# Kernel optimization log

Measured on AMD Instinct MI355X. Metric: run time of the kernel, lower is better.

The kernel has to match this reference:

```python
import jax, jax.numpy as jnp
import numpy as np

B_, L_, DM = 8, 1024, 256
DS, DC, EX = 16, 4, 2
DI = EX * DM            # d_inner = 512
DTR = max(1, DM // 16)  # dt_rank = 16


def setup_inputs() -> dict:
    key = jax.random.key(0)
    ks = iter(jax.random.split(key, 40))
    def n(shape, s=0.02):
        return jax.random.normal(next(ks), shape, jnp.float32) * s
    inp = {"x": jax.random.normal(next(ks), (B_, L_, DM), jnp.float32)}
    inp["norm_g"] = jnp.ones((DM,), jnp.float32)
    inp["norm_b"] = jnp.zeros((DM,), jnp.float32)
    for m in ("f", "b"):
        inp[f"inW_{m}"] = n((DM, 2 * DI))
        inp[f"convW_{m}"] = n((DI, DC))
        inp[f"convB_{m}"] = jnp.zeros((DI,), jnp.float32)
        inp[f"xW_{m}"] = n((DI, DTR + 2 * DS))
        inp[f"dtW_{m}"] = n((DTR, DI))
        inp[f"dtB_{m}"] = jnp.zeros((DI,), jnp.float32)
        # ALog init: log of [1..dState] repeated over dInner rows
        inp[f"ALog_{m}"] = jnp.log(jnp.tile(jnp.arange(1, DS + 1, dtype=jnp.float32), (DI, 1)))
        inp[f"Dp_{m}"] = jnp.ones((DI,), jnp.float32)
        inp[f"outW_{m}"] = n((DI, DM))
    inp["fusW"] = n((2 * DM, DM))
    inp["fusB"] = jnp.zeros((DM,), jnp.float32)
    return inp


def _dw_conv(x, w, b):
    # causal depthwise conv1d: x [B,L,DI], w [DI,DC] -> [B,L,DI]
    xc = jnp.transpose(x, (0, 2, 1))  # B,DI,L
    out = jax.lax.conv_general_dilated(
        xc, w[:, None, :], window_strides=(1,), padding=[(DC - 1, 0)],
        dimension_numbers=("NCH", "OIH", "NCH"), feature_group_count=DI)
    return jnp.transpose(out + b[:, None], (0, 2, 1))


def _ssm(x, xW, dtW, dtB, ALog, Dp):
    # x: [B,L,DI]
    A = -jnp.exp(ALog)                                   # [DI,DS]
    xdbl = x @ xW                                        # [B,L,DTR+2*DS]
    dlt, Bp, Cp = jnp.split(xdbl, [DTR, DTR + DS], axis=-1)
    delta = jax.nn.softplus(dlt @ dtW + dtB)             # [B,L,DI]
    dA = jnp.exp(delta[..., None] * A)                   # [B,L,DI,DS]
    dBx = (delta * x)[..., None] * Bp[:, :, None, :]     # [B,L,DI,DS]

    def step(h, t):
        a, bb, c = t
        h = a * h + bb                                   # [B,DI,DS]
        y = jnp.einsum('bdn,bn->bd', h, c)
        return h, y

    h0 = jnp.zeros((x.shape[0], DI, DS), x.dtype)
    _, ys = jax.lax.scan(step, h0, (jnp.moveaxis(dA, 1, 0),
                                    jnp.moveaxis(dBx, 1, 0),
                                    jnp.moveaxis(Cp, 1, 0)))
    return jnp.moveaxis(ys, 0, 1) + Dp * x               # [B,L,DI]


def _mamba(x, inW, convW, convB, xW, dtW, dtB, ALog, Dp, outW):
    xr = x @ inW                                         # [B,L,2*DI]
    xs, res = jnp.split(xr, 2, axis=-1)
    xs = jax.nn.silu(_dw_conv(xs, convW, convB))
    y = _ssm(xs, xW, dtW, dtB, ALog, Dp)
    return (y * jax.nn.silu(res)) @ outW                 # [B,L,DM]


def reference(x, norm_g, norm_b,
              inW_f, convW_f, convB_f, xW_f, dtW_f, dtB_f, ALog_f, Dp_f, outW_f,
              inW_b, convW_b, convB_b, xW_b, dtW_b, dtB_b, ALog_b, Dp_b, outW_b,
              fusW, fusB):
    # LayerNorm
    mu = x.mean(-1, keepdims=True)
    var = ((x - mu) ** 2).mean(-1, keepdims=True)
    xn = (x - mu) * jax.lax.rsqrt(var + 1e-5) * norm_g + norm_b
    # forward-direction Mamba
    xf = _mamba(xn, inW_f, convW_f, convB_f, xW_f, dtW_f, dtB_f, ALog_f, Dp_f, outW_f)
    # backward-direction Mamba (flip along time)
    xb = _mamba(jnp.flip(xn, 1), inW_b, convW_b, convB_b, xW_b, dtW_b, dtB_b, ALog_b, Dp_b, outW_b)
    xb = jnp.flip(xb, 1)
    fused = jnp.concatenate([xf, xb], axis=-1) @ fusW + fusB
    return x + fused  # dropout is identity in eval
```

## Files before the change

### kernel.cpp

```cpp
#include <hip/hip_runtime.h>
#include <cmath>

typedef __bf16 bf16x8 __attribute__((ext_vector_type(8)));
typedef float  f32x4  __attribute__((ext_vector_type(4)));
typedef float  f32x2  __attribute__((ext_vector_type(2)));

#define B_  8
#define L_  1024
#define DM  256
#define DI  512
#define DS  16
#define DTR 16
#define M_  (B_*L_)
#define NC  64
#define CT  16

__device__ inline float softplus_f(float z){
  return (z > 20.f) ? z : __logf(1.f + __expf(z));
}
__device__ inline float silu_f(float z){
  return z / (1.f + __expf(-z));
}

__device__ inline void pow_tree(float e1, float* p){
  float e2=e1*e1, e4=e2*e2, e8=e4*e4;
  float e3=e2*e1, e5=e4*e1, e6=e4*e2, e7=e4*e3;
  p[0]=e1;  p[1]=e2;  p[2]=e3;  p[3]=e4;
  p[4]=e5;  p[5]=e6;  p[6]=e7;  p[7]=e8;
  p[8]=e8*e1;  p[9]=e8*e2;  p[10]=e8*e3;  p[11]=e8*e4;
  p[12]=e8*e5; p[13]=e8*e6; p[14]=e8*e7;  p[15]=e8*e8;
}

__device__ inline int flag_from_x(const void* x){
  const unsigned short* u = (const unsigned short*)x;
  int lane = threadIdx.x & 63;
  unsigned short v = u[2*lane];
  int e = (v >> 7) & 0xFF;
  unsigned long long m = __ballot(e >= 160 || e < 96);
  return __popcll(m) > 16;
}

struct PrepJob { const void* src; void* dst; int rows; int cols; int f32out; };
struct PrepArgs { PrepJob j[26]; int nj; };

__global__ __launch_bounds__(256) void prep_k(PrepArgs a, const void* xsrc){
  const int f = flag_from_x(xsrc);
  int e = blockIdx.x*256 + threadIdx.x;
  #pragma unroll 1
  for (int jj=0; jj<a.nj; jj++){
    int sz = a.j[jj].rows * a.j[jj].cols;
    if (e < sz){
      int cols = a.j[jj].cols;
      int r = e / cols, c = e - r*cols;
      float v = f ? ((const float*)a.j[jj].src)[e] : (float)((const __bf16*)a.j[jj].src)[e];
      if (a.j[jj].f32out) ((float*)a.j[jj].dst)[c*a.j[jj].rows + r] = v;
      else ((__bf16*)a.j[jj].dst)[(long)c*a.j[jj].rows + r] = (__bf16)v;
      return;
    }
    e -= sz;
  }
}

__global__ __launch_bounds__(256) void ln_k(const void* x, const __bf16* g,
                                            const __bf16* bb, __bf16* xn){
  const int f = flag_from_x(x);
  const int row = blockIdx.x;
  const int d = threadIdx.x;
  long idx = (long)row*DM + d;
  float v = f ? ((const float*)x)[idx] : (float)(((const __bf16*)x)[idx]);
  float s = v, q = v*v;
  #pragma unroll
  for (int off=32; off>0; off>>=1){
    s += __shfl_down(s, off);
    q += __shfl_down(q, off);
  }
  __shared__ float ss[4], sq[4];
  int w = d >> 6, ln = d & 63;
  if (ln == 0){ ss[w] = s; sq[w] = q; }
  __syncthreads();
  s = ss[0]+ss[1]+ss[2]+ss[3];
  q = sq[0]+sq[1]+sq[2]+sq[3];
  float mu  = s * (1.f/DM);
  float var = q * (1.f/DM) - mu*mu;
  float xnv = (v - mu) * rsqrtf(var + 1e-5f) * (float)g[d] + (float)bb[d];
  xn[idx] = (__bf16)xnv;
}

template<int BM,int BN,int KK>
__global__ __launch_bounds__(256) void gemm_in_k(
    const __bf16* A, const __bf16* B0, const __bf16* B1,
    __bf16* xz0, __bf16* xz1, __bf16* res0, __bf16* res1,
    int lda, int ldb)
{
  constexpr int TM = BM/2, TN = BN/2;
  constexpr int WMT = TM/16, WNT = TN/16;
  constexpr int LA = BM/64, LB = BN/64;

  const int dir = blockIdx.z;
  const __bf16* Bt = dir ? B1 : B0;
  __bf16* xz  = dir ? xz1 : xz0;
  __bf16* res = dir ? res1 : res0;
  const int tid  = threadIdx.x;
  const int lane = tid & 63;
  const int wid  = tid >> 6;
  const int wm = wid & 1;
  const int wn = wid >> 1;
  const int mBase = blockIdx.x * BM;
  const int nBase = blockIdx.y * BN;
  const int lm = lane & 15;
  const int kq = (lane >> 4) * 8;

  __shared__ __bf16 As[BM*32];
  __shared__ __bf16 Bs[BN*32];

  const __bf16* aS[LA];
  const __bf16* bS[LB];
  {
    int colk = (tid & 3) * 8;
    #pragma unroll
    for (int ld=0; ld<LA; ld++){
      int r = mBase + ld*64 + (tid >> 2);
      if (dir==1){ int b = r >> 10, t = r & (L_-1); r = (b<<10) + (L_-1-t); }
      aS[ld] = A + (long)r*lda + colk;
    }
    #pragma unroll
    for (int ld=0; ld<LB; ld++){
      int r = nBase + ld*64 + (tid >> 2);
      bS[ld] = Bt + (long)r*ldb + colk;
    }
  }

  f32x4 acc[WMT][WNT] = {};
  for (int k0=0; k0<KK; k0+=32){
    #pragma unroll
    for (int ld=0; ld<LA; ld++)
      __builtin_amdgcn_global_load_lds(
        (const __attribute__((address_space(1))) void*)(aS[ld] + k0),
        (__attribute__((address_space(3))) void*)(&As[ld*2048 + tid*8]), 16, 0, 0);
    #pragma unroll
    for (int ld=0; ld<LB; ld++)
      __builtin_amdgcn_global_load_lds(
        (const __attribute__((address_space(1))) void*)(bS[ld] + k0),
        (__attribute__((address_space(3))) void*)(&Bs[ld*2048 + tid*8]), 16, 0, 0);
    __syncthreads();
    bf16x8 af[WMT], bfr[WNT];
    #pragma unroll
    for (int i=0;i<WMT;i++) af[i]  = *(const bf16x8*)&As[(wm*TM + i*16 + lm)*32 + kq];
    #pragma unroll
    for (int j=0;j<WNT;j++) bfr[j] = *(const bf16x8*)&Bs[(wn*TN + j*16 + lm)*32 + kq];
    #pragma unroll
    for (int i=0;i<WMT;i++)
      #pragma unroll
      for (int j=0;j<WNT;j++)
        acc[i][j] = __builtin_amdgcn_mfma_f32_16x16x32_bf16(af[i], bfr[j], acc[i][j], 0,0,0);
    __syncthreads();
  }

  #pragma unroll
  for (int i=0;i<WMT;i++){
    #pragma unroll
    for (int rr=0;rr<4;rr++){
      int r = mBase + wm*TM + i*16 + (lane>>4)*4 + rr;
      #pragma unroll
      for (int j=0;j<WNT;j++){
        int c = nBase + wn*TN + j*16 + lm;
        float v = acc[i][j][rr];
        if (c < DI) xz[(long)r*DI + c] = (__bf16)v;
        else        res[(long)r*DI + (c-DI)] = (__bf16)v;
      }
    }
  }
}

template<int BM,int BN,int KK>
__global__ __launch_bounds__(256) void gemm_fin_k(
    const __bf16* Af, const __bf16* Ab,
    const __bf16* Bt0, const __bf16* Bt1,
    void* Cout, const __bf16* bias, const void* resid)
{
  constexpr int TM = BM/2, TN = BN/2;
  constexpr int WMT = TM/16, WNT = TN/16;
  constexpr int LA = BM/64, LB = BN/64;

  const int of = flag_from_x(resid);
  const int tid  = threadIdx.x;
  const int lane = tid & 63;
  const int wid  = tid >> 6;
  const int wm = wid & 1;
  const int wn = wid >> 1;
  const int mBase = blockIdx.x * BM;
  const int nBase = blockIdx.y * BN;
  const int lm = lane & 15;
  const int kq = (lane >> 4) * 8;

  __shared__ __bf16 As[BM*32];
  __shared__ __bf16 Bs[BN*32];

  f32x4 acc[WMT][WNT] = {};
  #pragma unroll 1
  for (int dd=0; dd<2; dd++){
    const __bf16* A  = dd ? Ab  : Af;
    const __bf16* Bt = dd ? Bt1 : Bt0;
    const __bf16* aS[LA];
    const __bf16* bS[LB];
    {
      int colk = (tid & 3) * 8;
      #pragma unroll
      for (int ld=0; ld<LA; ld++){
        int r = mBase + ld*64 + (tid >> 2);
        if (dd==1){ int b = r >> 10, t = r & (L_-1); r = (b<<10) + (L_-1-t); }
        aS[ld] = A + (long)r*DI + colk;
      }
      #pragma unroll
      for (int ld=0; ld<LB; ld++){
        int r = nBase + ld*64 + (tid >> 2);
        bS[ld] = Bt + (long)r*DI + colk;
      }
    }
    for (int k0=0; k0<KK; k0+=32){
      #pragma unroll
      for (int ld=0; ld<LA; ld++)
        __builtin_amdgcn_global_load_lds(
          (const __attribute__((address_space(1))) void*)(aS[ld] + k0),
          (__attribute__((address_space(3))) void*)(&As[ld*2048 + tid*8]), 16, 0, 0);
      #pragma unroll
      for (int ld=0; ld<LB; ld++)
        __builtin_amdgcn_global_load_lds(
          (const __attribute__((address_space(1))) void*)(bS[ld] + k0),
          (__attribute__((address_space(3))) void*)(&Bs[ld*2048 + tid*8]), 16, 0, 0);
      __syncthreads();
      bf16x8 af[WMT], bfr[WNT];
      #pragma unroll
      for (int i=0;i<WMT;i++) af[i]  = *(const bf16x8*)&As[(wm*TM + i*16 + lm)*32 + kq];
      #pragma unroll
      for (int j=0;j<WNT;j++) bfr[j] = *(const bf16x8*)&Bs[(wn*TN + j*16 + lm)*32 + kq];
      #pragma unroll
      for (int i=0;i<WMT;i++)
        #pragma unroll
        for (int j=0;j<WNT;j++)
          acc[i][j] = __builtin_amdgcn_mfma_f32_16x16x32_bf16(af[i], bfr[j], acc[i][j], 0,0,0);
      __syncthreads();
    }
  }

  #pragma unroll
  for (int i=0;i<WMT;i++){
    #pragma unroll
    for (int rr=0;rr<4;rr++){
      int r = mBase + wm*TM + i*16 + (lane>>4)*4 + rr;
      #pragma unroll
      for (int j=0;j<WNT;j++){
        int c = nBase + wn*TN + j*16 + lm;
        float v = acc[i][j][rr];
        float rsd = of ? ((const float*)resid)[(long)r*DM + c]
                       : (float)((const __bf16*)resid)[(long)r*DM + c];
        v += (float)bias[c] + rsd;
        if (of) ((float*)Cout)[(long)r*DM + c] = v;
        else    ((__bf16*)Cout)[(long)r*DM + c] = (__bf16)v;
      }
    }
  }
}

template<int WMT,int WNT,int BWM,int BWN,int KK>
__global__ __launch_bounds__(64*BWM*BWN) void gemm_r_k(
    const __bf16* A0, const __bf16* A1,
    const __bf16* B0, const __bf16* B1,
    __bf16* C0, __bf16* C1,
    int lda, int ldb, int ldc)
{
  const int dir = blockIdx.z;
  const __bf16* A  = dir ? A1 : A0;
  const __bf16* Bt = dir ? B1 : B0;
  __bf16* C = dir ? C1 : C0;
  const int tid  = threadIdx.x;
  const int lane = tid & 63;
  const int wid  = tid >> 6;
  const int wm = wid % BWM;
  const int wn = wid / BWM;
  const int mBase = (blockIdx.x*BWM + wm) * (WMT*16);
  const int nBase = (blockIdx.y*BWN + wn) * (WNT*16);
  const int lm = lane & 15;
  const int kq = (lane >> 4) * 8;

  long aoff[WMT];
  #pragma unroll
  for (int i=0;i<WMT;i++) aoff[i] = (long)(mBase + i*16 + lm) * lda + kq;
  long boff[WNT];
  #pragma unroll
  for (int j=0;j<WNT;j++) boff[j] = (long)(nBase + j*16 + lm) * ldb + kq;

  f32x4 acc[WMT][WNT] = {};
  #pragma unroll
  for (int k0=0; k0<KK; k0+=32){
    bf16x8 af[WMT], bfr[WNT];
    #pragma unroll
    for (int i=0;i<WMT;i++) af[i]  = *(const bf16x8*)(A  + aoff[i] + k0);
    #pragma unroll
    for (int j=0;j<WNT;j++) bfr[j] = *(const bf16x8*)(Bt + boff[j] + k0);
    #pragma unroll
    for (int i=0;i<WMT;i++)
      #pragma unroll
      for (int j=0;j<WNT;j++)
        acc[i][j] = __builtin_amdgcn_mfma_f32_16x16x32_bf16(af[i], bfr[j], acc[i][j], 0,0,0);
  }

  #pragma unroll
  for (int i=0;i<WMT;i++)
    #pragma unroll
    for (int rr=0;rr<4;rr++){
      int r = mBase + i*16 + (lane>>4)*4 + rr;
      #pragma unroll
      for (int j=0;j<WNT;j++){
        int c = nBase + j*16 + lm;
        C[(long)r*ldc + c] = (__bf16)acc[i][j][rr];
      }
    }
}

__global__ __launch_bounds__(256) void xproj_k(
    const __bf16* xs0, const __bf16* xs1,
    const __bf16* B0, const __bf16* B1,
    float* xd0, float* xd1)
{
  const int dir = blockIdx.z;
  const __bf16* A  = dir ? xs1 : xs0;
  const __bf16* Bt = dir ? B1 : B0;
  float* C = dir ? xd1 : xd0;
  const int tid  = threadIdx.x;
  const int lane = tid & 63;
  const int wid  = tid >> 6;
  const int mBase = blockIdx.x*64 + wid*16;
  const int kc = blockIdx.y * 128;
  const int lm = lane & 15;
  const int kq = (lane >> 4) * 8;

  long aoff = (long)(mBase + lm)*DI + kc + kq;
  long boff[3];
  #pragma unroll
  for (int j=0;j<3;j++) boff[j] = (long)(j*16 + lm)*DI + kc + kq;

  f32x4 acc[3] = {};
  #pragma unroll
  for (int k0=0; k0<128; k0+=32){
    bf16x8 af = *(const bf16x8*)(A + aoff + k0);
    bf16x8 bfr[3];
    #pragma unroll
    for (int j=0;j<3;j++) bfr[j] = *(const bf16x8*)(Bt + boff[j] + k0);
    #pragma unroll
    for (int j=0;j<3;j++)
      acc[j] = __builtin_amdgcn_mfma_f32_16x16x32_bf16(af, bfr[j], acc[j], 0,0,0);
  }

  #pragma unroll
  for (int rr=0;rr<4;rr++){
    int r = mBase + (lane>>4)*4 + rr;
    #pragma unroll
    for (int j=0;j<3;j++){
      int c = j*16 + lm;
      atomicAdd(&C[(long)r*48 + c], acc[j][rr]);
    }
  }
}

__global__ __launch_bounds__(256) void conv_k(
    const __bf16* xz0, const __bf16* xz1,
    const float* cw0, const float* cw1,
    const __bf16* cb0, const __bf16* cb1,
    __bf16* xs0, __bf16* xs1)
{
  const int dir = blockIdx.z;
  const __bf16* xz = dir ? xz1 : xz0;
  const float*  cw = dir ? cw1 : cw0;
  const __bf16* cb = dir ? cb1 : cb0;
  __bf16* xs = dir ? xs1 : xs0;

  int gid = blockIdx.x*256 + threadIdx.x;
  int c8 = gid & 63;
  int t  = (gid >> 6) & (L_-1);
  int b  = gid >> 16;
  int cbase = c8*8;

  float acc[8];
  bf16x8 bb = *(const bf16x8*)(cb + cbase);
  #pragma unroll
  for (int c=0;c<8;c++) acc[c] = (float)bb[c];
  #pragma unroll
  for (int j=0;j<4;j++){
    int tj = t - 3 + j;
    if (tj >= 0){
      bf16x8 xv = *(const bf16x8*)(xz + ((long)(b*L_ + tj))*DI + cbase);
      #pragma unroll
      for (int c=0;c<8;c++) acc[c] += (float)xv[c] * cw[j*DI + cbase + c];
    }
  }
  bf16x8 outv;
  #pragma unroll
  for (int c=0;c<8;c++) outv[c] = (__bf16)silu_f(acc[c]);
  *(bf16x8*)(xs + ((long)(b*L_ + t))*DI + cbase) = outv;
}

__global__ __launch_bounds__(256) void dt_k(
    const float* xd0, const float* xd1,
    const float* dw0, const float* dw1,
    const __bf16* dtB0, const __bf16* dtB1,
    float* dg0, float* dg1)
{
  const int dir = blockIdx.z;
  const float*  xd  = dir ? xd1 : xd0;
  const float*  dw  = dir ? dw1 : dw0;
  const __bf16* dtB = dir ? dtB1 : dtB0;
  float* dg = dir ? dg1 : dg0;
  const long row0 = (long)blockIdx.x * 32;
  const int tid = threadIdx.x;

  __shared__ float sdlt[32][16];
  { int e = tid*2; int r = e>>4, q = e&15;
    *(f32x2*)&sdlt[r][q] = *(const f32x2*)(xd + (row0+r)*48 + q); }

  const int d0 = tid, d1 = tid + 256;
  float dwa[16], dwb[16];
  { const f32x4* p = (const f32x4*)(dw + d0*DTR);
    #pragma unroll
    for (int q=0;q<4;q++){ f32x4 v=p[q]; dwa[q*4]=v[0]; dwa[q*4+1]=v[1]; dwa[q*4+2]=v[2]; dwa[q*4+3]=v[3]; } }
  { const f32x4* p = (const f32x4*)(dw + d1*DTR);
    #pragma unroll
    for (int q=0;q<4;q++){ f32x4 v=p[q]; dwb[q*4]=v[0]; dwb[q*4+1]=v[1]; dwb[q*4+2]=v[2]; dwb[q*4+3]=v[3]; } }
  const float b0v = (float)dtB[d0];
  const float b1v = (float)dtB[d1];
  __syncthreads();

  #pragma unroll 4
  for (int r=0;r<32;r++){
    f32x4 q0 = *(const f32x4*)&sdlt[r][0];
    f32x4 q1 = *(const f32x4*)&sdlt[r][4];
    f32x4 q2 = *(const f32x4*)&sdlt[r][8];
    f32x4 q3 = *(const f32x4*)&sdlt[r][12];
    float z0 = b0v, z1 = b1v;
    z0 += q0[0]*dwa[0]+q0[1]*dwa[1]+q0[2]*dwa[2]+q0[3]*dwa[3];
    z0 += q1[0]*dwa[4]+q1[1]*dwa[5]+q1[2]*dwa[6]+q1[3]*dwa[7];
    z0 += q2[0]*dwa[8]+q2[1]*dwa[9]+q2[2]*dwa[10]+q2[3]*dwa[11];
    z0 += q3[0]*dwa[12]+q3[1]*dwa[13]+q3[2]*dwa[14]+q3[3]*dwa[15];
    z1 += q0[0]*dwb[0]+q0[1]*dwb[1]+q0[2]*dwb[2]+q0[3]*dwb[3];
    z1 += q1[0]*dwb[4]+q1[1]*dwb[5]+q1[2]*dwb[6]+q1[3]*dwb[7];
    z1 += q2[0]*dwb[8]+q2[1]*dwb[9]+q2[2]*dwb[10]+q2[3]*dwb[11];
    z1 += q3[0]*dwb[12]+q3[1]*dwb[13]+q3[2]*dwb[14]+q3[3]*dwb[15];
    dg[(row0+r)*DI + d0] = softplus_f(z0);
    dg[(row0+r)*DI + d1] = softplus_f(z1);
  }
}

__global__ __launch_bounds__(256) void scanA_k(
    const float* xd0, const float* xd1,
    const __bf16* xs0, const __bf16* xs1,
    const float* dg0, const float* dg1,
    const float* ALf0, const float* ALf1,
    float* hend, float* sumd)
{
  const int dir = blockIdx.z;
  const float*  xd  = dir ? xd1 : xd0;
  const __bf16* xs  = dir ? xs1 : xs0;
  const float*  dg  = dir ? dg1 : dg0;
  const float*  ALf = dir ? ALf1 : ALf0;

  const int b   = blockIdx.y;
  const int c   = blockIdx.x >> 1;
  const int dg_ = blockIdx.x & 1;
  const int tid = threadIdx.x;
  const int d   = dg_*256 + tid;
  const int db  = dir*8 + b;
  const long row0 = (long)b*L_ + c*CT;

  __shared__ float sB[CT][16];
  if (tid < CT*4){ int e = tid*4; int t = e>>4, n = e&15;
    *(f32x4*)&sB[t][n] = *(const f32x4*)(xd + (row0+t)*48 + 16 + n); }

  float A[16];
  { const f32x4* p = (const f32x4*)(ALf + d*DS);
    #pragma unroll
    for (int q=0;q<4;q++){ f32x4 v=p[q];
      A[q*4]=-__expf(v[0]); A[q*4+1]=-__expf(v[1]); A[q*4+2]=-__expf(v[2]); A[q*4+3]=-__expf(v[3]); } }
  bool pow_ok = true;
  #pragma unroll
  for (int n=0;n<16;n++) pow_ok = pow_ok && (fabsf(A[n] + (float)(n+1)) < 0.003f*(n+1));

  float h[16];
  #pragma unroll
  for (int n=0;n<16;n++) h[n]=0.f;
  float sdelta = 0.f;
  __syncthreads();

  if (pow_ok){
    #pragma unroll 2
    for (int t=0;t<CT;t++){
      long row = row0 + t;
      f32x4 b0 = *(const f32x4*)&sB[t][0];
      f32x4 b1 = *(const f32x4*)&sB[t][4];
      f32x4 b2 = *(const f32x4*)&sB[t][8];
      f32x4 b3 = *(const f32x4*)&sB[t][12];
      float delta = dg[row*DI + d];
      sdelta += delta;
      float xv = (float)xs[row*DI + d];
      float dx = delta*xv;
      float pw[16];
      pow_tree(__expf(-delta), pw);
      float Bv[16] = {b0[0],b0[1],b0[2],b0[3], b1[0],b1[1],b1[2],b1[3],
                      b2[0],b2[1],b2[2],b2[3], b3[0],b3[1],b3[2],b3[3]};
      #pragma unroll
      for (int n=0;n<16;n++)
        h[n] = pw[n]*h[n] + dx*Bv[n];
    }
  } else {
    #pragma unroll 2
    for (int t=0;t<CT;t++){
      long row = row0 + t;
      f32x4 b0 = *(const f32x4*)&sB[t][0];
      f32x4 b1 = *(const f32x4*)&sB[t][4];
      f32x4 b2 = *(const f32x4*)&sB[t][8];
      f32x4 b3 = *(const f32x4*)&sB[t][12];
      float delta = dg[row*DI + d];
      sdelta += delta;
      float xv = (float)xs[row*DI + d];
      float dx = delta*xv;
      float Bv[16] = {b0[0],b0[1],b0[2],b0[3], b1[0],b1[1],b1[2],b1[3],
                      b2[0],b2[1],b2[2],b2[3], b3[0],b3[1],b3[2],b3[3]};
      #pragma unroll
      for (int n=0;n<16;n++)
        h[n] = __expf(delta*A[n])*h[n] + dx*Bv[n];
    }
  }

  long hb = (((long)db*NC + c)*DI + d)*16;
  f32x4* hp = (f32x4*)(hend + hb);
  #pragma unroll
  for (int q=0;q<4;q++){ f32x4 v; v[0]=h[q*4]; v[1]=h[q*4+1]; v[2]=h[q*4+2]; v[3]=h[q*4+3]; hp[q]=v; }
  sumd[((long)db*NC + c)*DI + d] = sdelta;
}

__global__ __launch_bounds__(256) void scanB_k(
    const float* ALf0, const float* ALf1,
    const float* hend, const float* sumd, float* Hbuf)
{
  int gid = blockIdx.x*256 + threadIdx.x;
  int n  = gid & 15;
  int d  = (gid>>4) & 511;
  int db = gid >> 13;
  const float* ALf = (db>=8) ? ALf1 : ALf0;
  float A_dn = -__expf(ALf[d*DS + n]);
  float H = 0.f;
  #pragma unroll 1
  for (int c=0;c<NC;c++){
    long base = (((long)db*NC + c)*DI + d)*16 + n;
    Hbuf[base] = H;
    float S = sumd[((long)db*NC + c)*DI + d];
    H = hend[base] + __expf(A_dn*S)*H;
  }
}

__global__ __launch_bounds__(256) void scanC_k(
    const float* xd0, const float* xd1,
    const __bf16* xs0, const __bf16* xs1,
    __bf16* res0, __bf16* res1,
    const float* dg0, const float* dg1,
    const float* ALf0, const float* ALf1,
    const __bf16* Dp0, const __bf16* Dp1,
    const float* Hbuf)
{
  const int dir = blockIdx.z;
  const float*  xd  = dir ? xd1 : xd0;
  const __bf16* xs  = dir ? xs1 : xs0;
  __bf16*       res = dir ? res1 : res0;
  const float*  dg  = dir ? dg1 : dg0;
  const float*  ALf = dir ? ALf1 : ALf0;
  const __bf16* Dp  = dir ? Dp1 : Dp0;

  const int b   = blockIdx.y;
  const int c   = blockIdx.x >> 1;
  const int dg_ = blockIdx.x & 1;
  const int tid = threadIdx.x;
  const int d   = dg_*256 + tid;
  const int db  = dir*8 + b;
  const long row0 = (long)b*L_ + c*CT;

  __shared__ float sBC[CT][32];
  if (tid < CT*8){ int e = tid*4; int t = e>>5, cc = e&31;
    *(f32x4*)&sBC[t][cc] = *(const f32x4*)(xd + (row0+t)*48 + 16 + cc); }

  float A[16];
  { const f32x4* p = (const f32x4*)(ALf + d*DS);
    #pragma unroll
    for (int q=0;q<4;q++){ f32x4 v=p[q];
      A[q*4]=-__expf(v[0]); A[q*4+1]=-__expf(v[1]); A[q*4+2]=-__expf(v[2]); A[q*4+3]=-__expf(v[3]); } }
  bool pow_ok = true;
  #pragma unroll
  for (int n=0;n<16;n++) pow_ok = pow_ok && (fabsf(A[n] + (float)(n+1)) < 0.003f*(n+1));

  float h[16];
  { long hb = (((long)db*NC + c)*DI + d)*16;
    const f32x4* p = (const f32x4*)(Hbuf + hb);
    #pragma unroll
    for (int q=0;q<4;q++){ f32x4 v = p[q]; h[q*4]=v[0]; h[q*4+1]=v[1]; h[q*4+2]=v[2]; h[q*4+3]=v[3]; } }
  const float Dpv = (float)Dp[d];
  __syncthreads();

  if (pow_ok){
    #pragma unroll 2
    for (int t=0;t<CT;t++){
      long row = row0 + t;
      f32x4 b0 = *(const f32x4*)&sBC[t][0];
      f32x4 b1 = *(const f32x4*)&sBC[t][4];
      f32x4 b2 = *(const f32x4*)&sBC[t][8];
      f32x4 b3 = *(const f32x4*)&sBC[t][12];
      f32x4 c0 = *(const f32x4*)&sBC[t][16];
      f32x4 c1 = *(const f32x4*)&sBC[t][20];
      f32x4 c2 = *(const f32x4*)&sBC[t][24];
      f32x4 c3 = *(const f32x4*)&sBC[t][28];
      float delta = dg[row*DI + d];
      float xv = (float)xs[row*DI + d];
      float dx = delta*xv;
      float pw[16];
      pow_tree(__expf(-delta), pw);
      float Bv[16] = {b0[0],b0[1],b0[2],b0[3], b1[0],b1[1],b1[2],b1[3],
                      b2[0],b2[1],b2[2],b2[3], b3[0],b3[1],b3[2],b3[3]};
      float Cv[16] = {c0[0],c0[1],c0[2],c0[3], c1[0],c1[1],c1[2],c1[3],
                      c2[0],c2[1],c2[2],c2[3], c3[0],c3[1],c3[2],c3[3]};
      float p = 0.f;
      #pragma unroll
      for (int n=0;n<16;n++){
        h[n] = pw[n]*h[n] + dx*Bv[n];
        p += h[n]*Cv[n];
      }
      float yv = p + Dpv*xv;
      float rv = (float)res[row*DI + d];
      res[row*DI + d] = (__bf16)(yv * silu_f(rv));
    }
  } else {
    #pragma unroll 2
    for (int t=0;t<CT;t++){
      long row = row0 + t;
      f32x4 b0 = *(const f32x4*)&sBC[t][0];
      f32x4 b1 = *(const f32x4*)&sBC[t][4];
      f32x4 b2 = *(const f32x4*)&sBC[t][8];
      f32x4 b3 = *(const f32x4*)&sBC[t][12];
      f32x4 c0 = *(const f32x4*)&sBC[t][16];
      f32x4 c1 = *(const f32x4*)&sBC[t][20];
      f32x4 c2 = *(const f32x4*)&sBC[t][24];
      f32x4 c3 = *(const f32x4*)&sBC[t][28];
      float delta = dg[row*DI + d];
      float xv = (float)xs[row*DI + d];
      float dx = delta*xv;
      float Bv[16] = {b0[0],b0[1],b0[2],b0[3], b1[0],b1[1],b1[2],b1[3],
                      b2[0],b2[1],b2[2],b2[3], b3[0],b3[1],b3[2],b3[3]};
      float Cv[16] = {c0[0],c0[1],c0[2],c0[3], c1[0],c1[1],c1[2],c1[3],
                      c2[0],c2[1],c2[2],c2[3], c3[0],c3[1],c3[2],c3[3]};
      float p = 0.f;
      #pragma unroll
      for (int n=0;n<16;n++){
        h[n] = __expf(delta*A[n])*h[n] + dx*Bv[n];
        p += h[n]*Cv[n];
      }
      float yv = p + Dpv*xv;
      float rv = (float)res[row*DI + d];
      res[row*DI + d] = (__bf16)(yv * silu_f(rv));
    }
  }
}

extern "C" void kernel_launch(void* const* d_in, const int* in_sizes, int n_in,
                              void* d_out, int out_size, void* d_ws, size_t ws_size,
                              hipStream_t stream)
{
  const size_t MB = 1u<<20;
  if (ws_size < 160*MB) return;

  char* w = (char*)d_ws;
  __bf16* xz[2]  = {(__bf16*)(w + 0),      (__bf16*)(w + 8*MB)};
  __bf16* res[2] = {(__bf16*)(w + 16*MB),  (__bf16*)(w + 24*MB)};
  __bf16* xsc[2] = {(__bf16*)(w + 32*MB),  (__bf16*)(w + 40*MB)};
  __bf16* xn     = (__bf16*)(w + 48*MB);
  float*  xdbl[2]= {(float*)(w + 48*MB),   (float*)(w + 48*MB + (size_t)M_*48*4)};

  char* wp = w + 52*MB;
  auto carve = [&](size_t bytes)->void*{
    void* p = wp;
    wp += (bytes + 255) & ~(size_t)255;
    return p;
  };
  __bf16 *inWt[2], *xWt[2], *outWr[2], *BtC[2];
  float *dtWt[2], *convWt[2];
  for (int m=0;m<2;m++){
    inWt[m]   = (__bf16*)carve((size_t)(2*DI)*DM*2);
    xWt[m]    = (__bf16*)carve((size_t)48*DI*2);
    outWr[m]  = (__bf16*)carve((size_t)DI*DM*2);
    BtC[m]    = (__bf16*)carve((size_t)DM*DI*2);
    dtWt[m]   = (float*)carve((size_t)DI*DTR*4);
    convWt[m] = (float*)carve((size_t)4*DI*4);
  }
  __bf16* fusWt = (__bf16*)carve((size_t)DM*(2*DM)*2);
  float* ALf[2] = {(float*)carve((size_t)DI*DS*4), (float*)carve((size_t)DI*DS*4)};

  char* cp = w + 57*MB;
  auto carve2 = [&](size_t elems)->__bf16*{
    __bf16* p = (__bf16*)cp;
    cp += (elems*2 + 255) & ~(size_t)255;
    return p;
  };
  __bf16* ngc = carve2(DM);
  __bf16* nbc = carve2(DM);
  __bf16 *convBc[2], *dtBc[2], *Dpc[2];
  for (int m=0;m<2;m++){
    convBc[m] = carve2(DI);
    dtBc[m]   = carve2(DI);
    Dpc[m]    = carve2(DI);
  }
  __bf16* fusBc = carve2(DM);

  float* dgA[2] = {(float*)(w + 58*MB), (float*)(w + 74*MB)};
  float* hend = (float*)(w + 90*MB);
  float* sumd = (float*)(w + 124*MB);
  float* Hbuf = (float*)(w + 127*MB);

  PrepArgs pa;
  int ji = 0;
  size_t tot = 0;
  auto addj = [&](const void* s, void* dst, int rows, int cols, int f32o){
    pa.j[ji++] = {s, dst, rows, cols, f32o};
    tot += (size_t)rows*cols;
  };
  for (int m=0;m<2;m++){
    int base = 3 + m*9;
    addj(d_in[base+0], inWt[m],  DM,  2*DI, 0);
    addj(d_in[base+3], xWt[m],   DI,  48,   0);
    addj(d_in[base+8], outWr[m], 1,   DI*DM,0);
    addj(d_in[base+4], dtWt[m],  DTR, DI,   1);
    addj(d_in[base+1], convWt[m],DI,  4,    1);
    addj(d_in[base+2], convBc[m],1, DI, 0);
    addj(d_in[base+5], dtBc[m],  1, DI, 0);
    addj(d_in[base+6], (void*)ALf[m], 1, DI*DS, 1);
    addj(d_in[base+7], Dpc[m],   1, DI, 0);
  }
  addj(d_in[21], fusWt, 2*DM, DM, 0);
  addj(d_in[1],  ngc, 1, DM, 0);
  addj(d_in[2],  nbc, 1, DM, 0);
  addj(d_in[22], fusBc, 1, DM, 0);
  pa.nj = ji;
  prep_k<<<(int)((tot+255)/256), 256, 0, stream>>>(pa, d_in[0]);

  gemm_r_k<1,4,4,1,DM><<<dim3(4, 8, 2), 256, 0, stream>>>(
      fusWt, fusWt + DM, outWr[0], outWr[1], BtC[0], BtC[1], 2*DM, DM, DI);

  ln_k<<<M_, 256, 0, stream>>>(d_in[0], ngc, nbc, xn);
  gemm_in_k<128,128,256><<<dim3(M_/128, (2*DI)/128, 2), 256, 0, stream>>>(
      xn, inWt[0], inWt[1], xz[0], xz[1], res[0], res[1], DM, DM);
  conv_k<<<dim3((M_*64)/256, 1, 2), 256, 0, stream>>>(
      xz[0], xz[1], convWt[0], convWt[1], convBc[0], convBc[1], xsc[0], xsc[1]);

  hipMemsetAsync(w + 48*MB, 0, (size_t)M_*48*4*2, stream);
  xproj_k<<<dim3(M_/64, 4, 2), 256, 0, stream>>>(
      xsc[0], xsc[1], xWt[0], xWt[1], xdbl[0], xdbl[1]);

  dt_k<<<dim3(M_/32, 1, 2), 256, 0, stream>>>(
      xdbl[0], xdbl[1], dtWt[0], dtWt[1], dtBc[0], dtBc[1], dgA[0], dgA[1]);
  scanA_k<<<dim3(NC*2, B_, 2), 256, 0, stream>>>(
      xdbl[0], xdbl[1], xsc[0], xsc[1], dgA[0], dgA[1], ALf[0], ALf[1], hend, sumd);
  scanB_k<<<131072/256, 256, 0, stream>>>(ALf[0], ALf[1], hend, sumd, Hbuf);
  scanC_k<<<dim3(NC*2, B_, 2), 256, 0, stream>>>(
      xdbl[0], xdbl[1], xsc[0], xsc[1], res[0], res[1],
      dgA[0], dgA[1], ALf[0], ALf[1], Dpc[0], Dpc[1], Hbuf);

  gemm_fin_k<64,64,DI><<<dim3(M_/64, DM/64, 1), 256, 0, stream>>>(
      res[0], res[1], BtC[0], BtC[1], d_out, fusBc, d_in[0]);
}
```

Measured before the change: 285.6 us.

## Fuse dt projection into scan kernels, merge LN with weight fold, drop atomics

Result: faster. 276.0 us (-3.3%).

```diff
diff --git a/kernel.cpp b/kernel.cpp
--- a/kernel.cpp
+++ b/kernel.cpp
@@ -2,6 +2,7 @@
 #include <cmath>
 
 typedef __bf16 bf16x8 __attribute__((ext_vector_type(8)));
+typedef __bf16 bf16x4 __attribute__((ext_vector_type(4)));
 typedef float  f32x4  __attribute__((ext_vector_type(4)));
 typedef float  f32x2  __attribute__((ext_vector_type(2)));
 
@@ -61,29 +62,76 @@
   }
 }
 
-__global__ __launch_bounds__(256) void ln_k(const void* x, const __bf16* g,
-                                            const __bf16* bb, __bf16* xn){
-  const int f = flag_from_x(x);
-  const int row = blockIdx.x;
-  const int d = threadIdx.x;
-  long idx = (long)row*DM + d;
-  float v = f ? ((const float*)x)[idx] : (float)(((const __bf16*)x)[idx]);
-  float s = v, q = v*v;
-  #pragma unroll
-  for (int off=32; off>0; off>>=1){
-    s += __shfl_down(s, off);
-    q += __shfl_down(q, off);
-  }
-  __shared__ float ss[4], sq[4];
-  int w = d >> 6, ln = d & 63;
-  if (ln == 0){ ss[w] = s; sq[w] = q; }
-  __syncthreads();
-  s = ss[0]+ss[1]+ss[2]+ss[3];
-  q = sq[0]+sq[1]+sq[2]+sq[3];
-  float mu  = s * (1.f/DM);
-  float var = q * (1.f/DM) - mu*mu;
-  float xnv = (v - mu) * rsqrtf(var + 1e-5f) * (float)g[d] + (float)bb[d];
-  xn[idx] = (__bf16)xnv;
+__global__ __launch_bounds__(256) void lnw_k(
+    const void* x, const __bf16* g, const __bf16* bb, __bf16* xn,
+    const __bf16* fusWt, const __bf16* outWr0, const __bf16* outWr1,
+    __bf16* BtC0, __bf16* BtC1)
+{
+  const int bx = blockIdx.x;
+  const int tid = threadIdx.x;
+  const int lane = tid & 63;
+  const int wid = tid >> 6;
+
+  if (bx < M_/4){
+    const int f = flag_from_x(x);
+    long row = (long)bx*4 + wid;
+    long base = row*DM + lane*4;
+    float v0,v1,v2,v3;
+    if (f){ f32x4 xv = *(const f32x4*)((const float*)x + base);
+            v0=xv[0]; v1=xv[1]; v2=xv[2]; v3=xv[3]; }
+    else  { bf16x4 xv = *(const bf16x4*)((const __bf16*)x + base);
+            v0=(float)xv[0]; v1=(float)xv[1]; v2=(float)xv[2]; v3=(float)xv[3]; }
+    float s = v0+v1+v2+v3;
+    float q = v0*v0+v1*v1+v2*v2+v3*v3;
+    #pragma unroll
+    for (int off=32; off>0; off>>=1){ s += __shfl_xor(s,off); q += __shfl_xor(q,off); }
+    float mu = s*(1.f/DM), var = q*(1.f/DM)-mu*mu;
+    float rs = rsqrtf(var+1e-5f);
+    bf16x4 gv = *(const bf16x4*)(g + lane*4);
+    bf16x4 bv = *(const bf16x4*)(bb + lane*4);
+    bf16x4 o;
+    o[0]=(__bf16)((v0-mu)*rs*(float)gv[0]+(float)bv[0]);
+    o[1]=(__bf16)((v1-mu)*rs*(float)gv[1]+(float)bv[1]);
+    o[2]=(__bf16)((v2-mu)*rs*(float)gv[2]+(float)bv[2]);
+    o[3]=(__bf16)((v3-mu)*rs*(float)gv[3]+(float)bv[3]);
+    *(bf16x4*)(xn + base) = o;
+  } else {
+    int b2 = bx - M_/4;
+    int wz  = b2 >> 5;
+    int rem = b2 & 31;
+    int gx = rem & 3, gy = rem >> 2;
+    const __bf16* A  = fusWt + wz*DM;
+    const __bf16* Bt = wz ? outWr1 : outWr0;
+    __bf16* C = wz ? BtC1 : BtC0;
+    const int mBase = (gx*4 + wid)*16;
+    const int nBase = gy*64;
+    const int lm = lane & 15;
+    const int kq = (lane >> 4)*8;
+    long aoff = (long)(mBase+lm)*(2*DM) + kq;
+    long boff[4];
+    #pragma unroll
+    for (int j=0;j<4;j++) boff[j] = (long)(nBase+j*16+lm)*DM + kq;
+    f32x4 acc[4] = {};
+    #pragma unroll
+    for (int k0=0;k0<DM;k0+=32){
+      bf16x8 af = *(const bf16x8*)(A + aoff + k0);
+      bf16x8 bfr[4];
+      #pragma unroll
+      for (int j=0;j<4;j++) bfr[j] = *(const bf16x8*)(Bt + boff[j] + k0);
+      #pragma unroll
+      for (int j=0;j<4;j++)
+        acc[j] = __builtin_amdgcn_mfma_f32_16x16x32_bf16(af, bfr[j], acc[j], 0,0,0);
+    }
+    #pragma unroll
+    for (int rr=0;rr<4;rr++){
+      int r = mBase + (lane>>4)*4 + rr;
+      #pragma unroll
+      for (int j=0;j<4;j++){
+        int c = nBase + j*16 + lm;
+        C[(long)r*DI + c] = (__bf16)acc[j][rr];
+      }
+    }
+  }
 }
 
 template<int BM,int BN,int KK>
@@ -266,13 +314,13 @@
 __global__ __launch_bounds__(64*BWM*BWN) void gemm_r_k(
     const __bf16* A0, const __bf16* A1,
     const __bf16* B0, const __bf16* B1,
-    __bf16* C0, __bf16* C1,
+    float* C0, float* C1,
     int lda, int ldb, int ldc)
 {
   const int dir = blockIdx.z;
   const __bf16* A  = dir ? A1 : A0;
   const __bf16* Bt = dir ? B1 : B0;
-  __bf16* C = dir ? C1 : C0;
+  float* C = dir ? C1 : C0;
   const int tid  = threadIdx.x;
   const int lane = tid & 63;
   const int wid  = tid >> 6;
@@ -313,54 +361,9 @@
       #pragma unroll
       for (int j=0;j<WNT;j++){
         int c = nBase + j*16 + lm;
-        C[(long)r*ldc + c] = (__bf16)acc[i][j][rr];
+        C[(long)r*ldc + c] = acc[i][j][rr];
       }
     }
-}
-
-__global__ __launch_bounds__(256) void xproj_k(
-    const __bf16* xs0, const __bf16* xs1,
-    const __bf16* B0, const __bf16* B1,
-    float* xd0, float* xd1)
-{
-  const int dir = blockIdx.z;
-  const __bf16* A  = dir ? xs1 : xs0;
-  const __bf16* Bt = dir ? B1 : B0;
-  float* C = dir ? xd1 : xd0;
-  const int tid  = threadIdx.x;
-  const int lane = tid & 63;
-  const int wid  = tid >> 6;
-  const int mBase = blockIdx.x*64 + wid*16;
-  const int kc = blockIdx.y * 128;
-  const int lm = lane & 15;
-  const int kq = (lane >> 4) * 8;
-
-  long aoff = (long)(mBase + lm)*DI + kc + kq;
-  long boff[3];
-  #pragma unroll
-  for (int j=0;j<3;j++) boff[j] = (long)(j*16 + lm)*DI + kc + kq;
-
-  f32x4 acc[3] = {};
-  #pragma unroll
-  for (int k0=0; k0<128; k0+=32){
-    bf16x8 af = *(const bf16x8*)(A + aoff + k0);
-    bf16x8 bfr[3];
-    #pragma unroll
-    for (int j=0;j<3;j++) bfr[j] = *(const bf16x8*)(Bt + boff[j] + k0);
-    #pragma unroll
-    for (int j=0;j<3;j++)
-      acc[j] = __builtin_amdgcn_mfma_f32_16x16x32_bf16(af, bfr[j], acc[j], 0,0,0);
-  }
-
-  #pragma unroll
-  for (int rr=0;rr<4;rr++){
-    int r = mBase + (lane>>4)*4 + rr;
-    #pragma unroll
-    for (int j=0;j<3;j++){
-      int c = j*16 + lm;
-      atomicAdd(&C[(long)r*48 + c], acc[j][rr]);
-    }
-  }
 }
 
 __global__ __launch_bounds__(256) void conv_k(
@@ -400,67 +403,19 @@
   *(bf16x8*)(xs + ((long)(b*L_ + t))*DI + cbase) = outv;
 }
 
-__global__ __launch_bounds__(256) void dt_k(
-    const float* xd0, const float* xd1,
-    const float* dw0, const float* dw1,
-    const __bf16* dtB0, const __bf16* dtB1,
-    float* dg0, float* dg1)
-{
-  const int dir = blockIdx.z;
-  const float*  xd  = dir ? xd1 : xd0;
-  const float*  dw  = dir ? dw1 : dw0;
-  const __bf16* dtB = dir ? dtB1 : dtB0;
-  float* dg = dir ? dg1 : dg0;
-  const long row0 = (long)blockIdx.x * 32;
-  const int tid = threadIdx.x;
-
-  __shared__ float sdlt[32][16];
-  { int e = tid*2; int r = e>>4, q = e&15;
-    *(f32x2*)&sdlt[r][q] = *(const f32x2*)(xd + (row0+r)*48 + q); }
-
-  const int d0 = tid, d1 = tid + 256;
-  float dwa[16], dwb[16];
-  { const f32x4* p = (const f32x4*)(dw + d0*DTR);
-    #pragma unroll
-    for (int q=0;q<4;q++){ f32x4 v=p[q]; dwa[q*4]=v[0]; dwa[q*4+1]=v[1]; dwa[q*4+2]=v[2]; dwa[q*4+3]=v[3]; } }
-  { const f32x4* p = (const f32x4*)(dw + d1*DTR);
-    #pragma unroll
-    for (int q=0;q<4;q++){ f32x4 v=p[q]; dwb[q*4]=v[0]; dwb[q*4+1]=v[1]; dwb[q*4+2]=v[2]; dwb[q*4+3]=v[3]; } }
-  const float b0v = (float)dtB[d0];
-  const float b1v = (float)dtB[d1];
-  __syncthreads();
-
-  #pragma unroll 4
-  for (int r=0;r<32;r++){
-    f32x4 q0 = *(const f32x4*)&sdlt[r][0];
-    f32x4 q1 = *(const f32x4*)&sdlt[r][4];
-    f32x4 q2 = *(const f32x4*)&sdlt[r][8];
-    f32x4 q3 = *(const f32x4*)&sdlt[r][12];
-    float z0 = b0v, z1 = b1v;
-    z0 += q0[0]*dwa[0]+q0[1]*dwa[1]+q0[2]*dwa[2]+q0[3]*dwa[3];
-    z0 += q1[0]*dwa[4]+q1[1]*dwa[5]+q1[2]*dwa[6]+q1[3]*dwa[7];
-    z0 += q2[0]*dwa[8]+q2[1]*dwa[9]+q2[2]*dwa[10]+q2[3]*dwa[11];
-    z0 += q3[0]*dwa[12]+q3[1]*dwa[13]+q3[2]*dwa[14]+q3[3]*dwa[15];
-    z1 += q0[0]*dwb[0]+q0[1]*dwb[1]+q0[2]*dwb[2]+q0[3]*dwb[3];
-    z1 += q1[0]*dwb[4]+q1[1]*dwb[5]+q1[2]*dwb[6]+q1[3]*dwb[7];
-    z1 += q2[0]*dwb[8]+q2[1]*dwb[9]+q2[2]*dwb[10]+q2[3]*dwb[11];
-    z1 += q3[0]*dwb[12]+q3[1]*dwb[13]+q3[2]*dwb[14]+q3[3]*dwb[15];
-    dg[(row0+r)*DI + d0] = softplus_f(z0);
-    dg[(row0+r)*DI + d1] = softplus_f(z1);
-  }
-}
-
 __global__ __launch_bounds__(256) void scanA_k(
     const float* xd0, const float* xd1,
     const __bf16* xs0, const __bf16* xs1,
-    const float* dg0, const float* dg1,
+    const float* dw0, const float* dw1,
+    const __bf16* dtB0, const __bf16* dtB1,
     const float* ALf0, const float* ALf1,
     float* hend, float* sumd)
 {
   const int dir = blockIdx.z;
   const float*  xd  = dir ? xd1 : xd0;
   const __bf16* xs  = dir ? xs1 : xs0;
-  const float*  dg  = dir ? dg1 : dg0;
+  const float*  dw  = dir ? dw1 : dw0;
+  const __bf16* dtB = dir ? dtB1 : dtB0;
   const float*  ALf = dir ? ALf1 : ALf0;
 
   const int b   = blockIdx.y;
@@ -471,10 +426,14 @@
   const int db  = dir*8 + b;
   const long row0 = (long)b*L_ + c*CT;
 
-  __shared__ float sB[CT][16];
-  if (tid < CT*4){ int e = tid*4; int t = e>>4, n = e&15;
-    *(f32x4*)&sB[t][n] = *(const f32x4*)(xd + (row0+t)*48 + 16 + n); }
-
+  __shared__ float sAB[CT][32];
+  if (tid < CT*8){ int e = tid*4; int t = e>>5, cc = e&31;
+    *(f32x4*)&sAB[t][cc] = *(const f32x4*)(xd + (row0+t)*48 + cc); }
+
+  float dwq[16];
+  { const f32x4* p = (const f32x4*)(dw + d*DTR);
+    #pragma unroll
+    for (int q=0;q<4;q++){ f32x4 v=p[q]; dwq[q*4]=v[0]; dwq[q*4+1]=v[1]; dwq[q*4+2]=v[2]; dwq[q*4+3]=v[3]; } }
   float A[16];
   { const f32x4* p = (const f32x4*)(ALf + d*DS);
     #pragma unroll
@@ -483,6 +442,7 @@
   bool pow_ok = true;
   #pragma unroll
   for (int n=0;n<16;n++) pow_ok = pow_ok && (fabsf(A[n] + (float)(n+1)) < 0.003f*(n+1));
+  const float dtbv = (float)dtB[d];
 
   float h[16];
   #pragma unroll
@@ -493,14 +453,22 @@
   if (pow_ok){
     #pragma unroll 2
     for (int t=0;t<CT;t++){
-      long row = row0 + t;
-      f32x4 b0 = *(const f32x4*)&sB[t][0];
-      f32x4 b1 = *(const f32x4*)&sB[t][4];
-      f32x4 b2 = *(const f32x4*)&sB[t][8];
-      f32x4 b3 = *(const f32x4*)&sB[t][12];
-      float delta = dg[row*DI + d];
+      f32x4 q0 = *(const f32x4*)&sAB[t][0];
+      f32x4 q1 = *(const f32x4*)&sAB[t][4];
+      f32x4 q2 = *(const f32x4*)&sAB[t][8];
+      f32x4 q3 = *(const f32x4*)&sAB[t][12];
+      f32x4 b0 = *(const f32x4*)&sAB[t][16];
+      f32x4 b1 = *(const f32x4*)&sAB[t][20];
+      f32x4 b2 = *(const f32x4*)&sAB[t][24];
+      f32x4 b3 = *(const f32x4*)&sAB[t][28];
+      float z = dtbv;
+      z += q0[0]*dwq[0]+q0[1]*dwq[1]+q0[2]*dwq[2]+q0[3]*dwq[3];
+      z += q1[0]*dwq[4]+q1[1]*dwq[5]+q1[2]*dwq[6]+q1[3]*dwq[7];
+      z += q2[0]*dwq[8]+q2[1]*dwq[9]+q2[2]*dwq[10]+q2[3]*dwq[11];
+      z += q3[0]*dwq[12]+q3[1]*dwq[13]+q3[2]*dwq[14]+q3[3]*dwq[15];
+      float delta = softplus_f(z);
       sdelta += delta;
-      float xv = (float)xs[row*DI + d];
+      float xv = (float)xs[(row0+t)*DI + d];
       float dx = delta*xv;
       float pw[16];
       pow_tree(__expf(-delta), pw);
@@ -513,14 +481,22 @@
   } else {
     #pragma unroll 2
     for (int t=0;t<CT;t++){
-      long row = row0 + t;
-      f32x4 b0 = *(const f32x4*)&sB[t][0];
-      f32x4 b1 = *(const f32x4*)&sB[t][4];
-      f32x4 b2 = *(const f32x4*)&sB[t][8];
-      f32x4 b3 = *(const f32x4*)&sB[t][12];
-      float delta = dg[row*DI + d];
+      f32x4 q0 = *(const f32x4*)&sAB[t][0];
+      f32x4 q1 = *(const f32x4*)&sAB[t][4];
+      f32x4 q2 = *(const f32x4*)&sAB[t][8];
+      f32x4 q3 = *(const f32x4*)&sAB[t][12];
+      f32x4 b0 = *(const f32x4*)&sAB[t][16];
+      f32x4 b1 = *(const f32x4*)&sAB[t][20];
+      f32x4 b2 = *(const f32x4*)&sAB[t][24];
+      f32x4 b3 = *(const f32x4*)&sAB[t][28];
+      float z = dtbv;
+      z += q0[0]*dwq[0]+q0[1]*dwq[1]+q0[2]*dwq[2]+q0[3]*dwq[3];
+      z += q1[0]*dwq[4]+q1[1]*dwq[5]+q1[2]*dwq[6]+q1[3]*dwq[7];
+      z += q2[0]*dwq[8]+q2[1]*dwq[9]+q2[2]*dwq[10]+q2[3]*dwq[11];
+      z += q3[0]*dwq[12]+q3[1]*dwq[13]+q3[2]*dwq[14]+q3[3]*dwq[15];
+      float delta = softplus_f(z);
       sdelta += delta;
-      float xv = (float)xs[row*DI + d];
+      float xv = (float)xs[(row0+t)*DI + d];
       float dx = delta*xv;
       float Bv[16] = {b0[0],b0[1],b0[2],b0[3], b1[0],b1[1],b1[2],b1[3],
                       b2[0],b2[1],b2[2],b2[3], b3[0],b3[1],b3[2],b3[3]};
@@ -561,7 +537,8 @@
     const float* xd0, const float* xd1,
     const __bf16* xs0, const __bf16* xs1,
     __bf16* res0, __bf16* res1,
-    const float* dg0, const float* dg1,
+    const float* dw0, const float* dw1,
+    const __bf16* dtB0, const __bf16* dtB1,
     const float* ALf0, const float* ALf1,
     const __bf16* Dp0, const __bf16* Dp1,
     const float* Hbuf)
@@ -570,7 +547,8 @@
   const float*  xd  = dir ? xd1 : xd0;
   const __bf16* xs  = dir ? xs1 : xs0;
   __bf16*       res = dir ? res1 : res0;
-  const float*  dg  = dir ? dg1 : dg0;
+  const float*  dw  = dir ? dw1 : dw0;
+  const __bf16* dtB = dir ? dtB1 : dtB0;
   const float*  ALf = dir ? ALf1 : ALf0;
   const __bf16* Dp  = dir ? Dp1 : Dp0;
 
@@ -582,10 +560,14 @@
   const int db  = dir*8 + b;
   const long row0 = (long)b*L_ + c*CT;
 
-  __shared__ float sBC[CT][32];
-  if (tid < CT*8){ int e = tid*4; int t = e>>5, cc = e&31;
-    *(f32x4*)&sBC[t][cc] = *(const f32x4*)(xd + (row0+t)*48 + 16 + cc); }
-
+  __shared__ float sX[CT][48];
+  if (tid < CT*12){ int e = tid*4; int t = e/48, cc = e - t*48;
+    *(f32x4*)&sX[t][cc] = *(const f32x4*)(xd + (row0+t)*48 + cc); }
+
+  float dwq[16];
+  { const f32x4* p = (const f32x4*)(dw + d*DTR);
+    #pragma unroll
+    for (int q=0;q<4;q++){ f32x4 v=p[q]; dwq[q*4]=v[0]; dwq[q*4+1]=v[1]; dwq[q*4+2]=v[2]; dwq[q*4+3]=v[3]; } }
   float A[16];
   { const f32x4* p = (const f32x4*)(ALf + d*DS);
     #pragma unroll
@@ -594,6 +576,7 @@
   bool pow_ok = true;
   #pragma unroll
   for (int n=0;n<16;n++) pow_ok = pow_ok && (fabsf(A[n] + (float)(n+1)) < 0.003f*(n+1));
+  const float dtbv = (float)dtB[d];
 
   float h[16];
   { long hb = (((long)db*NC + c)*DI + d)*16;
@@ -607,15 +590,24 @@
     #pragma unroll 2
     for (int t=0;t<CT;t++){
       long row = row0 + t;
-      f32x4 b0 = *(const f32x4*)&sBC[t][0];
-      f32x4 b1 = *(const f32x4*)&sBC[t][4];
-      f32x4 b2 = *(const f32x4*)&sBC[t][8];
-      f32x4 b3 = *(const f32x4*)&sBC[t][12];
-      f32x4 c0 = *(const f32x4*)&sBC[t][16];
-      f32x4 c1 = *(const f32x4*)&sBC[t][20];
-      f32x4 c2 = *(const f32x4*)&sBC[t][24];
-      f32x4 c3 = *(const f32x4*)&sBC[t][28];
-      float delta = dg[row*DI + d];
+      f32x4 q0 = *(const f32x4*)&sX[t][0];
+      f32x4 q1 = *(const f32x4*)&sX[t][4];
+      f32x4 q2 = *(const f32x4*)&sX[t][8];
+      f32x4 q3 = *(const f32x4*)&sX[t][12];
+      f32x4 b0 = *(const f32x4*)&sX[t][16];
+      f32x4 b1 = *(const f32x4*)&sX[t][20];
+      f32x4 b2 = *(const f32x4*)&sX[t][24];
+      f32x4 b3 = *(const f32x4*)&sX[t][28];
+      f32x4 c0 = *(const f32x4*)&sX[t][32];
+      f32x4 c1 = *(const f32x4*)&sX[t][36];
+      f32x4 c2 = *(const f32x4*)&sX[t][40];
+      f32x4 c3 = *(const f32x4*)&sX[t][44];
+      float z = dtbv;
+      z += q0[0]*dwq[0]+q0[1]*dwq[1]+q0[2]*dwq[2]+q0[3]*dwq[3];
+      z += q1[0]*dwq[4]+q1[1]*dwq[5]+q1[2]*dwq[6]+q1[3]*dwq[7];
+      z += q2[0]*dwq[8]+q2[1]*dwq[9]+q2[2]*dwq[10]+q2[3]*dwq[11];
+      z += q3[0]*dwq[12]+q3[1]*dwq[13]+q3[2]*dwq[14]+q3[3]*dwq[15];
+      float delta = softplus_f(z);
       float xv = (float)xs[row*DI + d];
       float dx = delta*xv;
       float pw[16];
@@ -638,15 +630,24 @@
     #pragma unroll 2
     for (int t=0;t<CT;t++){
       long row = row0 + t;
-      f32x4 b0 = *(const f32x4*)&sBC[t][0];
-      f32x4 b1 = *(const f32x4*)&sBC[t][4];
-      f32x4 b2 = *(const f32x4*)&sBC[t][8];
-      f32x4 b3 = *(const f32x4*)&sBC[t][12];
-      f32x4 c0 = *(const f32x4*)&sBC[t][16];
-      f32x4 c1 = *(const f32x4*)&sBC[t][20];
-      f32x4 c2 = *(const f32x4*)&sBC[t][24];
-      f32x4 c3 = *(const f32x4*)&sBC[t][28];
-      float delta = dg[row*DI + d];
+      f32x4 q0 = *(const f32x4*)&sX[t][0];
+      f32x4 q1 = *(const f32x4*)&sX[t][4];
+      f32x4 q2 = *(const f32x4*)&sX[t][8];
+      f32x4 q3 = *(const f32x4*)&sX[t][12];
+      f32x4 b0 = *(const f32x4*)&sX[t][16];
+      f32x4 b1 = *(const f32x4*)&sX[t][20];
+      f32x4 b2 = *(const f32x4*)&sX[t][24];
+      f32x4 b3 = *(const f32x4*)&sX[t][28];
+      f32x4 c0 = *(const f32x4*)&sX[t][32];
+      f32x4 c1 = *(const f32x4*)&sX[t][36];
+      f32x4 c2 = *(const f32x4*)&sX[t][40];
+      f32x4 c3 = *(const f32x4*)&sX[t][44];
+      float z = dtbv;
+      z += q0[0]*dwq[0]+q0[1]*dwq[1]+q0[2]*dwq[2]+q0[3]*dwq[3];
+      z += q1[0]*dwq[4]+q1[1]*dwq[5]+q1[2]*dwq[6]+q1[3]*dwq[7];
+      z += q2[0]*dwq[8]+q2[1]*dwq[9]+q2[2]*dwq[10]+q2[3]*dwq[11];
+      z += q3[0]*dwq[12]+q3[1]*dwq[13]+q3[2]*dwq[14]+q3[3]*dwq[15];
+      float delta = softplus_f(z);
       float xv = (float)xs[row*DI + d];
       float dx = delta*xv;
       float Bv[16] = {b0[0],b0[1],b0[2],b0[3], b1[0],b1[1],b1[2],b1[3],
@@ -678,7 +679,7 @@
   __bf16* res[2] = {(__bf16*)(w + 16*MB),  (__bf16*)(w + 24*MB)};
   __bf16* xsc[2] = {(__bf16*)(w + 32*MB),  (__bf16*)(w + 40*MB)};
   __bf16* xn     = (__bf16*)(w + 48*MB);
-  float*  xdbl[2]= {(float*)(w + 48*MB),   (float*)(w + 48*MB + (size_t)M_*48*4)};
+  float*  xdbl[2]= {(float*)(w + 58*MB),   (float*)(w + 58*MB + (size_t)M_*48*4)};
 
   char* wp = w + 52*MB;
   auto carve = [&](size_t bytes)->void*{
@@ -715,7 +716,6 @@
   }
   __bf16* fusBc = carve2(DM);
 
-  float* dgA[2] = {(float*)(w + 58*MB), (float*)(w + 74*MB)};
   float* hend = (float*)(w + 90*MB);
   float* sumd = (float*)(w + 124*MB);
   float* Hbuf = (float*)(w + 127*MB);
@@ -746,27 +746,23 @@
   pa.nj = ji;
   prep_k<<<(int)((tot+255)/256), 256, 0, stream>>>(pa, d_in[0]);
 
-  gemm_r_k<1,4,4,1,DM><<<dim3(4, 8, 2), 256, 0, stream>>>(
-      fusWt, fusWt + DM, outWr[0], outWr[1], BtC[0], BtC[1], 2*DM, DM, DI);
-
-  ln_k<<<M_, 256, 0, stream>>>(d_in[0], ngc, nbc, xn);
+  lnw_k<<<M_/4 + 64, 256, 0, stream>>>(
+      d_in[0], ngc, nbc, xn, fusWt, outWr[0], outWr[1], BtC[0], BtC[1]);
+
   gemm_in_k<128,128,256><<<dim3(M_/128, (2*DI)/128, 2), 256, 0, stream>>>(
       xn, inWt[0], inWt[1], xz[0], xz[1], res[0], res[1], DM, DM);
   conv_k<<<dim3((M_*64)/256, 1, 2), 256, 0, stream>>>(
       xz[0], xz[1], convWt[0], convWt[1], convBc[0], convBc[1], xsc[0], xsc[1]);
-
-  hipMemsetAsync(w + 48*MB, 0, (size_t)M_*48*4*2, stream);
-  xproj_k<<<dim3(M_/64, 4, 2), 256, 0, stream>>>(
-      xsc[0], xsc[1], xWt[0], xWt[1], xdbl[0], xdbl[1]);
-
-  dt_k<<<dim3(M_/32, 1, 2), 256, 0, stream>>>(
-      xdbl[0], xdbl[1], dtWt[0], dtWt[1], dtBc[0], dtBc[1], dgA[0], dgA[1]);
+  gemm_r_k<1,3,4,1,DI><<<dim3(M_/64, 1, 2), 256, 0, stream>>>(
+      xsc[0], xsc[1], xWt[0], xWt[1], xdbl[0], xdbl[1], DI, DI, 48);
+
   scanA_k<<<dim3(NC*2, B_, 2), 256, 0, stream>>>(
-      xdbl[0], xdbl[1], xsc[0], xsc[1], dgA[0], dgA[1], ALf[0], ALf[1], hend, sumd);
+      xdbl[0], xdbl[1], xsc[0], xsc[1], dtWt[0], dtWt[1],
+      dtBc[0], dtBc[1], ALf[0], ALf[1], hend, sumd);
   scanB_k<<<131072/256, 256, 0, stream>>>(ALf[0], ALf[1], hend, sumd, Hbuf);
   scanC_k<<<dim3(NC*2, B_, 2), 256, 0, stream>>>(
       xdbl[0], xdbl[1], xsc[0], xsc[1], res[0], res[1],
-      dgA[0], dgA[1], ALf[0], ALf[1], Dpc[0], Dpc[1], Hbuf);
+      dtWt[0], dtWt[1], dtBc[0], dtBc[1], ALf[0], ALf[1], Dpc[0], Dpc[1], Hbuf);
 
   gemm_fin_k<64,64,DI><<<dim3(M_/64, DM/64, 1), 256, 0, stream>>>(
       res[0], res[1], BtC[0], BtC[1], d_out, fusBc, d_in[0]);
```
